# Kernel optimization log

Measured on AMD Instinct MI355X. Metric: run time of the kernel, lower is better.

## Reference

```python
import jax, jax.numpy as jnp
import numpy as np

U = 100001          # user_count = user_num + 1
I = 50001           # item_count = item_num + 1
N = U + I           # total nodes
D = 64              # embedding dim
E = 3_200_000       # user-item interactions
NNZ = 2 * E         # symmetric directed edges
N_LAYERS = 3


def setup_inputs() -> dict:
    key = jax.random.key(0)
    k1, k2, k3, k4 = jax.random.split(key, 4)
    user_emb = jax.random.normal(k1, (U, D), dtype=jnp.float32) * 0.1
    item_emb = jax.random.normal(k2, (I, D), dtype=jnp.float32) * 0.1
    # random bipartite interactions, symmetrized like _get_a_adj_matrix
    u = jax.random.randint(k3, (E,), 0, U, dtype=jnp.int32)
    it = jax.random.randint(k4, (E,), 0, I, dtype=jnp.int32)
    rows = jnp.concatenate([u, it + U])            # [NNZ]
    cols = jnp.concatenate([it + U, u])            # [NNZ]
    # D^{-1/2} A D^{-1/2}: deg from row sums of A (values are 1s, duplicates sum)
    deg = jax.ops.segment_sum(jnp.ones((NNZ,), jnp.float32), rows, num_segments=N) + 1e-7
    dinv = deg ** -0.5
    vals = dinv[rows] * dinv[cols]                 # [NNZ]
    return {"user_emb": user_emb, "item_emb": item_emb,
            "rows": rows, "cols": cols, "vals": vals}


def _spmm(rows, cols, vals, x):
    # out[r] += vals * x[c]  (COO SpMM via gather + segment_sum)
    return jax.ops.segment_sum(vals[:, None] * x[cols], rows, num_segments=N)


def reference(user_emb, item_emb, rows, cols, vals):
    all_emb = jnp.concatenate([user_emb, item_emb], axis=0)   # [N, D]
    acc = all_emb                                             # running sum over layers (== mean * (L+1))
    h = all_emb
    for _ in range(N_LAYERS):
        h = _spmm(rows, cols, vals, h)
        acc = acc + h
    out = acc / (N_LAYERS + 1)                                # mean over stacked layers
    return out[:U], out[U:]
```

## Files before the change

kernel.cpp:

```cpp
#include <hip/hip_runtime.h>
#include <hip/hip_fp16.h>

#define U_CNT 100001
#define I_CNT 50001
#define N_CNT 150002
#define DIM 64
#define BROWS 512
#define NB2 ((N_CNT + BROWS - 1) / BROWS)
#define NB2P 512
#define CH 8192

__device__ inline __half2 u2h(unsigned int u) { union { unsigned int u; __half2 h; } c; c.u = u; return c.h; }
__device__ inline unsigned int h2u(__half2 h) { union { unsigned int u; __half2 h; } c; c.h = h; return c.u; }

typedef float f4_t __attribute__((ext_vector_type(4)));
typedef unsigned int u4_t __attribute__((ext_vector_type(4)));

__device__ inline float4 ntload_f4(const float4* p) {
    f4_t v = __builtin_nontemporal_load((const f4_t*)p);
    return make_float4(v.x, v.y, v.z, v.w);
}
__device__ inline void ntstore_f4(float4* p, float4 v) {
    f4_t t; t.x = v.x; t.y = v.y; t.z = v.z; t.w = v.w;
    __builtin_nontemporal_store(t, (f4_t*)p);
}
__device__ inline void ntstore_u4(uint4* p, uint4 v) {
    u4_t t; t.x = v.x; t.y = v.y; t.z = v.z; t.w = v.w;
    __builtin_nontemporal_store(t, (u4_t*)p);
}

__global__ void bucket_hist(const int* __restrict__ rows, int* __restrict__ bhist,
                            int nnz) {
    __shared__ int lh[NB2];
    for (int i = threadIdx.x; i < NB2; i += blockDim.x) lh[i] = 0;
    __syncthreads();
    int stride = gridDim.x * blockDim.x;
    for (int i = blockIdx.x * blockDim.x + threadIdx.x; i < nnz; i += stride)
        atomicAdd(&lh[rows[i] >> 9], 1);
    __syncthreads();
    for (int i = threadIdx.x; i < NB2; i += blockDim.x) {
        int v = lh[i];
        if (v) atomicAdd(&bhist[i], v);
    }
}

__global__ void bucket_scan(const int* __restrict__ bhist,
                            int* __restrict__ bucket_ptr,
                            int* __restrict__ bcur) {
    __shared__ int sh[512];
    int t = threadIdx.x;
    int v0 = (t < NB2) ? bhist[t] : 0;
    sh[t] = v0;
    __syncthreads();
    for (int off = 1; off < 512; off <<= 1) {
        int v = (t >= off) ? sh[t - off] : 0;
        __syncthreads();
        sh[t] += v;
        __syncthreads();
    }
    if (t < NB2) {
        int ex = sh[t] - v0;
        bucket_ptr[t] = ex;
        bcur[t] = ex;
    }
    if (t == NB2 - 1) bucket_ptr[NB2] = sh[t];
}

__global__ void __launch_bounds__(256) partition_kernel(
    const int* __restrict__ rows, const int* __restrict__ cols,
    int* __restrict__ bcur, unsigned int* __restrict__ staging, int nnz)
{
    __shared__ int hist[NB2P];
    __shared__ int ofs[NB2 + 1];
    __shared__ int cur[NB2];
    __shared__ int gbase[NB2];
    __shared__ unsigned int recs[CH];
    __shared__ unsigned short guess[CH / 32];
    const int t = threadIdx.x;
    int base = blockIdx.x * CH;
    int lim = nnz - base; if (lim > CH) lim = CH;

    for (int i = t; i < NB2P; i += 256) hist[i] = 0;
    __syncthreads();
    for (int i = t; i < lim; i += 256)
        atomicAdd(&hist[rows[base + i] >> 9], 1);
    __syncthreads();
    for (int off = 1; off < NB2P; off <<= 1) {
        int v0 = (t >= off) ? hist[t - off] : 0;
        int i1 = t + 256;
        int v1 = hist[i1 - off];
        __syncthreads();
        hist[t] += v0;
        hist[i1] += v1;
        __syncthreads();
    }
    for (int i = t; i <= NB2; i += 256)
        ofs[i] = (i == 0) ? 0 : hist[i - 1];
    __syncthreads();
    for (int i = t; i < NB2; i += 256)
        cur[i] = ofs[i];
    for (int i = t; i < NB2; i += 256) {
        int lo_ = ofs[i], hi_ = ofs[i + 1];
        for (int m = (lo_ + 31) & ~31; m < hi_; m += 32)
            guess[m >> 5] = (unsigned short)i;
    }
    for (int i = t; i < NB2; i += 256) {
        int cnt = ofs[i + 1] - ofs[i];
        if (cnt) gbase[i] = atomicAdd(&bcur[i], cnt);
    }
    __syncthreads();
    for (int i = t; i < lim; i += 256) {
        int r = rows[base + i];
        int c = cols[base + i];
        int p = atomicAdd(&cur[r >> 9], 1);
        recs[p] = ((unsigned int)c << 9) | (unsigned int)(r & (BROWS - 1));
    }
    __syncthreads();
    for (int p = t; p < lim; p += 256) {
        unsigned int rec = recs[p];
        int lo = guess[p >> 5];
        while (ofs[lo + 1] <= p) ++lo;
        staging[gbase[lo] + (p - ofs[lo])] = rec;
    }
}

__global__ void binplace_kernel(const int* __restrict__ bucket_ptr,
                                const unsigned int* __restrict__ staging,
                                unsigned int* __restrict__ col_s,
                                int* __restrict__ row_ptr,
                                float* __restrict__ dinv) {
    __shared__ int hist[BROWS];
    __shared__ int cur[BROWS];
    int b = blockIdx.x;
    int base = b << 9;
    int beg = bucket_ptr[b];
    int end = bucket_ptr[b + 1];
    int t = threadIdx.x;
    hist[t] = 0;
    __syncthreads();
    for (int j = beg + t; j < end; j += BROWS)
        atomicAdd(&hist[staging[j] & (BROWS - 1u)], 1);
    __syncthreads();
    int cnt = hist[t];
    for (int off = 1; off < BROWS; off <<= 1) {
        int v = (t >= off) ? hist[t - off] : 0;
        __syncthreads();
        hist[t] += v;
        __syncthreads();
    }
    int start = beg + hist[t] - cnt;
    cur[t] = start;
    int r = base + t;
    if (r < N_CNT) {
        row_ptr[r] = start;
        dinv[r] = 1.0f / sqrtf((float)cnt + 1e-7f);
    }
    if (b == NB2 - 1 && t == 0) row_ptr[N_CNT] = end;
    __syncthreads();
    for (int j = beg + t; j < end; j += BROWS) {
        unsigned int rec = staging[j];
        int pos = atomicAdd(&cur[rec & (BROWS - 1u)], 1);
        col_s[pos] = rec >> 9;
    }
}

__global__ void init_kernel(const float4* __restrict__ ue,
                            const float4* __restrict__ ie,
                            const float* __restrict__ dinv,
                            uint4* __restrict__ hs) {
    int i = blockIdx.x * blockDim.x + threadIdx.x;
    if (i >= N_CNT * 8) return;
    int node = i >> 3;
    int s = i & 7;
    float d = dinv[node];
    size_t fo = (size_t)node * 16 + s * 2;
    float4 v0, v1;
    if (node < U_CNT) { v0 = ntload_f4(&ue[fo]); v1 = ntload_f4(&ue[fo + 1]); }
    else { size_t io = fo - (size_t)U_CNT * 16; v0 = ntload_f4(&ie[io]); v1 = ntload_f4(&ie[io + 1]); }
    uint4 h;
    h.x = h2u(__floats2half2_rn(d * v0.x, d * v0.y));
    h.y = h2u(__floats2half2_rn(d * v0.z, d * v0.w));
    h.z = h2u(__floats2half2_rn(d * v1.x, d * v1.y));
    h.w = h2u(__floats2half2_rn(d * v1.z, d * v1.w));
    hs[(size_t)node * 8 + s] = h;
}

__device__ inline void acc8(float4& a0, float4& a1, uint4 u) {
    float2 f;
    f = __half22float2(u2h(u.x)); a0.x += f.x; a0.y += f.y;
    f = __half22float2(u2h(u.y)); a0.z += f.x; a0.w += f.y;
    f = __half22float2(u2h(u.z)); a1.x += f.x; a1.y += f.y;
    f = __half22float2(u2h(u.w)); a1.z += f.x; a1.w += f.y;
}

__global__ void spmm_gather(const int* __restrict__ row_ptr,
                            const unsigned int* __restrict__ col_s,
                            const float* __restrict__ dinv,
                            const uint4* __restrict__ x,
                            uint4* __restrict__ y,
                            const uint4* __restrict__ h1s,
                            const float4* __restrict__ ue,
                            const float4* __restrict__ ie,
                            float4* __restrict__ acc,
                            int r0, int r1, int last) {
    int r = r0 + blockIdx.x * 32 + (threadIdx.x >> 3);
    int s = threadIdx.x & 7;
    if (r >= r1) return;
    int beg = row_ptr[r];
    int end = row_ptr[r + 1];
    float4 a0 = {0.f, 0.f, 0.f, 0.f}, a1 = {0.f, 0.f, 0.f, 0.f};
    float4 b0 = {0.f, 0.f, 0.f, 0.f}, b1 = {0.f, 0.f, 0.f, 0.f};
    int j = beg;
    for (; j + 4 <= end; j += 4) {
        unsigned int c0 = col_s[j];
        unsigned int c1 = col_s[j + 1];
        unsigned int c2 = col_s[j + 2];
        unsigned int c3 = col_s[j + 3];
        uint4 u0 = x[(size_t)c0 * 8 + s];
        uint4 u1 = x[(size_t)c1 * 8 + s];
        uint4 u2 = x[(size_t)c2 * 8 + s];
        uint4 u3 = x[(size_t)c3 * 8 + s];
        acc8(a0, a1, u0);
        acc8(b0, b1, u1);
        acc8(a0, a1, u2);
        acc8(b0, b1, u3);
    }
    for (; j < end; ++j) {
        unsigned int c0 = col_s[j];
        uint4 u0 = x[(size_t)c0 * 8 + s];
        acc8(a0, a1, u0);
    }
    a0.x += b0.x; a0.y += b0.y; a0.z += b0.z; a0.w += b0.w;
    a1.x += b1.x; a1.y += b1.y; a1.z += b1.z; a1.w += b1.w;

    float d = dinv[r];
    if (!last) {
        float d2 = d * d;
        uint4 h;
        h.x = h2u(__floats2half2_rn(d2 * a0.x, d2 * a0.y));
        h.y = h2u(__floats2half2_rn(d2 * a0.z, d2 * a0.w));
        h.z = h2u(__floats2half2_rn(d2 * a1.x, d2 * a1.y));
        h.w = h2u(__floats2half2_rn(d2 * a1.z, d2 * a1.w));
        ntstore_u4(&y[(size_t)r * 8 + s], h);
        return;
    }

    float inv = 1.0f / d;
    uint4 u1 = h1s[(size_t)r * 8 + s];
    uint4 u2v = x[(size_t)r * 8 + s];
    float4 s0 = {0.f, 0.f, 0.f, 0.f}, s1 = {0.f, 0.f, 0.f, 0.f};
    acc8(s0, s1, u1);
    acc8(s0, s1, u2v);
    size_t fo = (size_t)r * 16 + s * 2;
    float4 e0a, e0b;
    if (r < U_CNT) { e0a = ntload_f4(&ue[fo]); e0b = ntload_f4(&ue[fo + 1]); }
    else { size_t io = fo - (size_t)U_CNT * 16; e0a = ntload_f4(&ie[io]); e0b = ntload_f4(&ie[io + 1]); }
    float4 o0, o1;
    o0.x = 0.25f * (e0a.x + inv * s0.x + d * a0.x);
    o0.y = 0.25f * (e0a.y + inv * s0.y + d * a0.y);
    o0.z = 0.25f * (e0a.z + inv * s0.z + d * a0.z);
    o0.w = 0.25f * (e0a.w + inv * s0.w + d * a0.w);
    o1.x = 0.25f * (e0b.x + inv * s1.x + d * a1.x);
    o1.y = 0.25f * (e0b.y + inv * s1.y + d * a1.y);
    o1.z = 0.25f * (e0b.z + inv * s1.z + d * a1.z);
    o1.w = 0.25f * (e0b.w + inv * s1.w + d * a1.w);
    ntstore_f4(&acc[fo], o0);
    ntstore_f4(&acc[fo + 1], o1);
}

extern "C" void kernel_launch(void* const* d_in, const int* in_sizes, int n_in,
                              void* d_out, int out_size, void* d_ws, size_t ws_size,
                              hipStream_t stream) {
    const float* ue   = (const float*)d_in[0];
    const float* ie   = (const float*)d_in[1];
    const int*   rows = (const int*)d_in[2];
    const int*   cols = (const int*)d_in[3];
    int nnz = in_sizes[2];

    float* acc = (float*)d_out;

    unsigned int* ws = (unsigned int*)d_ws;
    uint4* hs0 = (uint4*)ws;
    uint4* hs1 = hs0 + (size_t)N_CNT * 8;
    int*   row_ptr    = (int*)(hs1 + (size_t)N_CNT * 8);
    int*   bhist      = row_ptr + (N_CNT + 1);
    int*   bucket_ptr = bhist + NB2;
    int*   bcur       = bucket_ptr + (NB2 + 1);
    float* dinv       = (float*)(bcur + NB2);
    unsigned int* staging = (unsigned int*)(dinv + N_CNT);
    unsigned int* col_s   = staging + nnz;

    const int tpb = 256;

    hipMemsetAsync(bhist, 0, NB2 * sizeof(int), stream);
    bucket_hist<<<512, tpb, 0, stream>>>(rows, bhist, nnz);
    bucket_scan<<<1, 512, 0, stream>>>(bhist, bucket_ptr, bcur);
    partition_kernel<<<(nnz + CH - 1) / CH, tpb, 0, stream>>>(
        rows, cols, bcur, staging, nnz);
    binplace_kernel<<<NB2, BROWS, 0, stream>>>(
        bucket_ptr, staging, col_s, row_ptr, dinv);

    init_kernel<<<(N_CNT * 8 + tpb - 1) / tpb, tpb, 0, stream>>>(
        (const float4*)ue, (const float4*)ie, dinv, hs0);

    uint4* cur_h = hs0;
    uint4* nxt_h = hs1;
    const int ublocks = (U_CNT + 31) / 32;
    const int iblocks = (N_CNT - U_CNT + 31) / 32;
    for (int l = 0; l < 3; ++l) {
        int last = (l == 2) ? 1 : 0;
        spmm_gather<<<ublocks, tpb, 0, stream>>>(
            row_ptr, col_s, dinv, cur_h, nxt_h, nxt_h,
            (const float4*)ue, (const float4*)ie, (float4*)acc, 0, U_CNT, last);
        spmm_gather<<<iblocks, tpb, 0, stream>>>(
            row_ptr, col_s, dinv, cur_h, nxt_h, nxt_h,
            (const float4*)ue, (const float4*)ie, (float4*)acc, U_CNT, N_CNT, last);
        uint4* tmp = cur_h; cur_h = nxt_h; nxt_h = tmp;
    }
}
```

Before: 592.9 us.

## Use smaller 128-row buckets and stage binplace output in shared memory

Shrinks the row buckets from 512 to 128 rows, so there are about 1172 buckets. The bucket scans in bucket_scan and partition_kernel become two-level scans (8 per thread plus a 256-wide scan), and the per-bucket cursor is dropped by counting down the inclusive prefix instead. binplace now builds each bucket's sorted column list in shared memory and writes it out coalesced, with a direct-write fallback for buckets over capacity. The aim is smaller, better-balanced binplace blocks and coalesced col_s writes, at the cost of more buckets, more shared memory in partition, and scattered staging writes split into more segments.

Result: no change. 587.6 us (-0.9%).

```diff
diff --git a/kernel.cpp b/kernel.cpp
--- a/kernel.cpp
+++ b/kernel.cpp
@@ -5,10 +5,11 @@
 #define I_CNT 50001
 #define N_CNT 150002
 #define DIM 64
-#define BROWS 512
+#define BROWS 128
 #define NB2 ((N_CNT + BROWS - 1) / BROWS)
-#define NB2P 512
+#define NB2R 1176
 #define CH 8192
+#define OUTCAP 10240
 
 __device__ inline __half2 u2h(unsigned int u) { union { unsigned int u; __half2 h; } c; c.u = u; return c.h; }
 __device__ inline unsigned int h2u(__half2 h) { union { unsigned int u; __half2 h; } c; c.h = h; return c.u; }
@@ -36,7 +37,7 @@
     __syncthreads();
     int stride = gridDim.x * blockDim.x;
     for (int i = blockIdx.x * blockDim.x + threadIdx.x; i < nnz; i += stride)
-        atomicAdd(&lh[rows[i] >> 9], 1);
+        atomicAdd(&lh[rows[i] >> 7], 1);
     __syncthreads();
     for (int i = threadIdx.x; i < NB2; i += blockDim.x) {
         int v = lh[i];
@@ -47,120 +48,167 @@
 __global__ void bucket_scan(const int* __restrict__ bhist,
                             int* __restrict__ bucket_ptr,
                             int* __restrict__ bcur) {
-    __shared__ int sh[512];
+    __shared__ int aux[256];
     int t = threadIdx.x;
-    int v0 = (t < NB2) ? bhist[t] : 0;
-    sh[t] = v0;
-    __syncthreads();
-    for (int off = 1; off < 512; off <<= 1) {
-        int v = (t >= off) ? sh[t - off] : 0;
-        __syncthreads();
-        sh[t] += v;
-        __syncthreads();
-    }
-    if (t < NB2) {
-        int ex = sh[t] - v0;
-        bucket_ptr[t] = ex;
-        bcur[t] = ex;
-    }
-    if (t == NB2 - 1) bucket_ptr[NB2] = sh[t];
+    int v[8];
+    int s = 0;
+    int b8 = t * 8;
+    if (t < 147) {
+        #pragma unroll
+        for (int k = 0; k < 8; ++k) {
+            int i = b8 + k;
+            int d = (i < NB2) ? bhist[i] : 0;
+            v[k] = s;
+            s += d;
+        }
+    }
+    aux[t] = s;
+    __syncthreads();
+    for (int off = 1; off < 256; off <<= 1) {
+        int x = (t >= off) ? aux[t - off] : 0;
+        __syncthreads();
+        aux[t] += x;
+        __syncthreads();
+    }
+    if (t < 147) {
+        int gb = (t > 0) ? aux[t - 1] : 0;
+        #pragma unroll
+        for (int k = 0; k < 8; ++k) {
+            int i = b8 + k;
+            if (i < NB2) {
+                int ex = gb + v[k];
+                bucket_ptr[i] = ex;
+                bcur[i] = ex;
+            }
+        }
+    }
+    if (t == 255) bucket_ptr[NB2] = aux[255];
 }
 
 __global__ void __launch_bounds__(256) partition_kernel(
     const int* __restrict__ rows, const int* __restrict__ cols,
     int* __restrict__ bcur, unsigned int* __restrict__ staging, int nnz)
 {
-    __shared__ int hist[NB2P];
+    __shared__ int hist[NB2R];
     __shared__ int ofs[NB2 + 1];
-    __shared__ int cur[NB2];
+    __shared__ int aux[256];
     __shared__ int gbase[NB2];
     __shared__ unsigned int recs[CH];
-    __shared__ unsigned short guess[CH / 32];
+    __shared__ unsigned short guess[CH / 8];
     const int t = threadIdx.x;
     int base = blockIdx.x * CH;
     int lim = nnz - base; if (lim > CH) lim = CH;
 
-    for (int i = t; i < NB2P; i += 256) hist[i] = 0;
+    for (int i = t; i < NB2R; i += 256) hist[i] = 0;
     __syncthreads();
     for (int i = t; i < lim; i += 256)
-        atomicAdd(&hist[rows[base + i] >> 9], 1);
-    __syncthreads();
-    for (int off = 1; off < NB2P; off <<= 1) {
-        int v0 = (t >= off) ? hist[t - off] : 0;
-        int i1 = t + 256;
-        int v1 = hist[i1 - off];
-        __syncthreads();
-        hist[t] += v0;
-        hist[i1] += v1;
-        __syncthreads();
-    }
-    for (int i = t; i <= NB2; i += 256)
-        ofs[i] = (i == 0) ? 0 : hist[i - 1];
-    __syncthreads();
-    for (int i = t; i < NB2; i += 256)
-        cur[i] = ofs[i];
+        atomicAdd(&hist[rows[base + i] >> 7], 1);
+    __syncthreads();
+    {
+        int s = 0;
+        if (t < 147) {
+            int b8 = t * 8;
+            #pragma unroll
+            for (int k = 0; k < 8; ++k) s += hist[b8 + k];
+        }
+        aux[t] = s;
+    }
+    __syncthreads();
+    for (int off = 1; off < 256; off <<= 1) {
+        int x = (t >= off) ? aux[t - off] : 0;
+        __syncthreads();
+        aux[t] += x;
+        __syncthreads();
+    }
+    if (t < 147) {
+        int run = (t > 0) ? aux[t - 1] : 0;
+        int b8 = t * 8;
+        #pragma unroll
+        for (int k = 0; k < 8; ++k) {
+            run += hist[b8 + k];
+            hist[b8 + k] = run;
+        }
+    }
+    __syncthreads();
+    if (t == 0) ofs[0] = 0;
+    for (int i = t; i < NB2; i += 256) ofs[i + 1] = hist[i];
+    __syncthreads();
     for (int i = t; i < NB2; i += 256) {
         int lo_ = ofs[i], hi_ = ofs[i + 1];
-        for (int m = (lo_ + 31) & ~31; m < hi_; m += 32)
-            guess[m >> 5] = (unsigned short)i;
-    }
-    for (int i = t; i < NB2; i += 256) {
-        int cnt = ofs[i + 1] - ofs[i];
+        for (int m = (lo_ + 7) & ~7; m < hi_; m += 8)
+            guess[m >> 3] = (unsigned short)i;
+        int cnt = hi_ - lo_;
         if (cnt) gbase[i] = atomicAdd(&bcur[i], cnt);
     }
     __syncthreads();
     for (int i = t; i < lim; i += 256) {
         int r = rows[base + i];
         int c = cols[base + i];
-        int p = atomicAdd(&cur[r >> 9], 1);
-        recs[p] = ((unsigned int)c << 9) | (unsigned int)(r & (BROWS - 1));
+        int p = atomicAdd(&hist[r >> 7], -1) - 1;
+        recs[p] = ((unsigned int)c << 7) | (unsigned int)(r & (BROWS - 1));
     }
     __syncthreads();
     for (int p = t; p < lim; p += 256) {
         unsigned int rec = recs[p];
-        int lo = guess[p >> 5];
+        int lo = guess[p >> 3];
         while (ofs[lo + 1] <= p) ++lo;
         staging[gbase[lo] + (p - ofs[lo])] = rec;
     }
 }
 
-__global__ void binplace_kernel(const int* __restrict__ bucket_ptr,
-                                const unsigned int* __restrict__ staging,
-                                unsigned int* __restrict__ col_s,
-                                int* __restrict__ row_ptr,
-                                float* __restrict__ dinv) {
+__global__ void __launch_bounds__(256) binplace_kernel(
+    const int* __restrict__ bucket_ptr,
+    const unsigned int* __restrict__ staging,
+    unsigned int* __restrict__ col_s,
+    int* __restrict__ row_ptr,
+    float* __restrict__ dinv) {
     __shared__ int hist[BROWS];
     __shared__ int cur[BROWS];
+    __shared__ unsigned int outb[OUTCAP];
     int b = blockIdx.x;
-    int base = b << 9;
+    int base = b << 7;
     int beg = bucket_ptr[b];
     int end = bucket_ptr[b + 1];
+    int total = end - beg;
     int t = threadIdx.x;
-    hist[t] = 0;
-    __syncthreads();
-    for (int j = beg + t; j < end; j += BROWS)
+    if (t < BROWS) hist[t] = 0;
+    __syncthreads();
+    for (int j = beg + t; j < end; j += 256)
         atomicAdd(&hist[staging[j] & (BROWS - 1u)], 1);
     __syncthreads();
-    int cnt = hist[t];
+    int cnt = (t < BROWS) ? hist[t] : 0;
     for (int off = 1; off < BROWS; off <<= 1) {
-        int v = (t >= off) ? hist[t - off] : 0;
-        __syncthreads();
-        hist[t] += v;
-        __syncthreads();
-    }
-    int start = beg + hist[t] - cnt;
-    cur[t] = start;
-    int r = base + t;
-    if (r < N_CNT) {
-        row_ptr[r] = start;
-        dinv[r] = 1.0f / sqrtf((float)cnt + 1e-7f);
+        int v = (t < BROWS && t >= off) ? hist[t - off] : 0;
+        __syncthreads();
+        if (t < BROWS) hist[t] += v;
+        __syncthreads();
+    }
+    if (t < BROWS) {
+        int startl = hist[t] - cnt;
+        cur[t] = startl;
+        int r = base + t;
+        if (r < N_CNT) {
+            row_ptr[r] = beg + startl;
+            dinv[r] = 1.0f / sqrtf((float)cnt + 1e-7f);
+        }
     }
     if (b == NB2 - 1 && t == 0) row_ptr[N_CNT] = end;
     __syncthreads();
-    for (int j = beg + t; j < end; j += BROWS) {
-        unsigned int rec = staging[j];
-        int pos = atomicAdd(&cur[rec & (BROWS - 1u)], 1);
-        col_s[pos] = rec >> 9;
+    if (total <= OUTCAP) {
+        for (int j = beg + t; j < end; j += 256) {
+            unsigned int rec = staging[j];
+            int pos = atomicAdd(&cur[rec & (BROWS - 1u)], 1);
+            outb[pos] = rec >> 7;
+        }
+        __syncthreads();
+        for (int k = t; k < total; k += 256)
+            col_s[beg + k] = outb[k];
+    } else {
+        for (int j = beg + t; j < end; j += 256) {
+            unsigned int rec = staging[j];
+            int pos = atomicAdd(&cur[rec & (BROWS - 1u)], 1);
+            col_s[beg + pos] = rec >> 7;
+        }
     }
 }
 
@@ -294,10 +342,10 @@
 
     hipMemsetAsync(bhist, 0, NB2 * sizeof(int), stream);
     bucket_hist<<<512, tpb, 0, stream>>>(rows, bhist, nnz);
-    bucket_scan<<<1, 512, 0, stream>>>(bhist, bucket_ptr, bcur);
+    bucket_scan<<<1, 256, 0, stream>>>(bhist, bucket_ptr, bcur);
     partition_kernel<<<(nnz + CH - 1) / CH, tpb, 0, stream>>>(
         rows, cols, bcur, staging, nnz);
-    binplace_kernel<<<NB2, BROWS, 0, stream>>>(
+    binplace_kernel<<<NB2, tpb, 0, stream>>>(
         bucket_ptr, staging, col_s, row_ptr, dinv);
 
     init_kernel<<<(N_CNT * 8 + tpb - 1) / tpb, tpb, 0, stream>>>(
```
